# Kernel optimization log

Hardware: AMD Instinct MI355X
Metric: run time of the kernel (lower is better)

The kernel has to match this reference:

```python
import jax, jax.numpy as jnp
import numpy as np

WIN = 12          # max_relative_position
HEAD_DIM = 64     # E, equals num_units of relative-position tables


def _rel_embed(table, length):
    r = jnp.arange(length)
    idx = jnp.clip(r[None, :] - r[:, None], -WIN, WIN) + WIN  # [L, L]
    return table[idx]  # [L, L, E]


def setup_inputs() -> dict:
    key = jax.random.key(0)
    ks = jax.random.split(key, 7)
    B, L, H, E = 4, 1024, 8, HEAD_DIM
    shp = (B, L, H, E)
    xavier = float(np.sqrt(6.0 / (2 * WIN + 1 + E)))
    return {
        "x": jax.random.normal(ks[0], shp, jnp.float32),
        "y": jax.random.normal(ks[1], shp, jnp.float32),
        "v_x": jax.random.normal(ks[2], shp, jnp.float32),
        "v_y": jax.random.normal(ks[3], shp, jnp.float32),
        "rel_k_table": jax.random.uniform(ks[4], (2 * WIN + 1, E), jnp.float32, -xavier, xavier),
        "rel_vx_table": jax.random.uniform(ks[5], (2 * WIN + 1, E), jnp.float32, -xavier, xavier),
        "rel_vy_table": jax.random.uniform(ks[6], (2 * WIN + 1, E), jnp.float32, -xavier, xavier),
        "attn_mask1": jnp.zeros((1,), jnp.bool_),
        "attn_mask2": jnp.zeros((1,), jnp.bool_),
    }


def reference(x, y, v_x, v_y, rel_k_table, rel_vx_table, rel_vy_table, attn_mask1, attn_mask2):
    B, L, H, E = x.shape
    scale = 1.0 / float(np.sqrt(E))

    rel_k = _rel_embed(rel_k_table, L)    # [L, L, E]
    rel_vy = _rel_embed(rel_vy_table, L)  # [L, L, E]
    rel_vx = _rel_embed(rel_vx_table, L)  # [L, L, E]

    # scores1[b,h,l,s] = <x_bl h, y_bs h> + <x_bl h, rel_k[l,s]>
    scores1 = jnp.einsum('blhe,bshe->bhls', x, y) \
            + jnp.einsum('blhe,lse->bhls', x, rel_k)
    scores2 = jnp.swapaxes(scores1, -2, -1)  # pre-softmax transpose

    A1 = jax.nn.softmax(scale * scores1, axis=-1)  # [B,H,L,S]
    A2 = jax.nn.softmax(scale * scores2, axis=-1)

    V_Y = jnp.einsum('bhls,bshd->bhld', A1, v_y) \
        + jnp.einsum('bhls,lsd->bhld', A1, rel_vy)
    V_X = jnp.einsum('bhls,bshd->bhld', A2, v_x) \
        + jnp.einsum('bhls,lsd->bhld', A2, rel_vx)

    # module returns (V_Y^T, None, V_X^T, None); drop the Nones
    return jnp.swapaxes(V_Y, 1, 2), jnp.swapaxes(V_X, 1, 2)
```

## Files before the change

kernel.cpp:

```cpp
#include <hip/hip_runtime.h>
#include <math.h>

#define LQ 1024
#define RS 512
#define PJ 26
#define NP 32
#define ASCALE 0.18033688f

typedef __attribute__((ext_vector_type(4))) float f32x4;
typedef __attribute__((ext_vector_type(8))) short short8x;

__device__ __forceinline__ unsigned pk2(float a, float b) {
  unsigned r;
  asm("v_cvt_pk_bf16_f32 %0, %1, %2" : "=v"(r) : "v"(a), "v"(b));
  return r;
}

__device__ __forceinline__ int swz(int row, int bc) {
  return row * 128 + (bc ^ ((row & 7) << 4));
}
__device__ __forceinline__ int swzVT(int row, int bc) {
  return row * 128 + (bc ^ ((((row >> 3) ^ row) & 7) << 4));
}

__global__ __launch_bounds__(256) void k_relproj(const float* __restrict__ x,
                                                 const float* __restrict__ relk,
                                                 float* __restrict__ P) {
  __shared__ float rk[25][68];
  __shared__ float xs[64][68];
  const int tid = threadIdx.x;
  const int pair = blockIdx.y, l0 = blockIdx.x * 64;
  const int b = pair >> 3, h = pair & 7;
  for (int i = tid; i < 25 * 64; i += 256) rk[i >> 6][i & 63] = relk[i] * ASCALE;
  const int row = tid >> 2, q = tid & 3;
  const float* xr = x + (size_t)b * 524288 + (size_t)(l0 + row) * RS + h * 64 + q * 16;
#pragma unroll
  for (int i = 0; i < 4; ++i) {
    float4 a = *(const float4*)(xr + i * 4);
    xs[row][q * 16 + i * 4 + 0] = a.x; xs[row][q * 16 + i * 4 + 1] = a.y;
    xs[row][q * 16 + i * 4 + 2] = a.z; xs[row][q * 16 + i * 4 + 3] = a.w;
  }
  __syncthreads();
  float* Pr = P + ((size_t)pair * LQ + l0 + row) * PJ;
  for (int j = q; j < 25; j += 4) {
    float acc = 0.f;
#pragma unroll
    for (int e = 0; e < 64; ++e) acc += xs[row][e] * rk[j][e];
    Pr[j] = acc;
  }
}

__global__ __launch_bounds__(256, 2) void k_fused(
    const float* __restrict__ x, const float* __restrict__ y,
    const float* __restrict__ vx, const float* __restrict__ vy,
    const float* __restrict__ relvx, const float* __restrict__ relvy,
    const float* __restrict__ P_g, float* __restrict__ out_g) {
  __shared__ __align__(16) char U[16384];
  __shared__ __align__(16) char Bb[2][8192];
  __shared__ __align__(16) char Vb[2][8192];
  __shared__ float W[128 * PJ];

  const int tid = threadIdx.x;
  const int p = blockIdx.x;
  const int g = p & 63, bx = p >> 6;
  const int pair = g & 31, mode = g >> 5;
  const int b = pair >> 3, h = pair & 7;
  const int l0 = bx * 128;

  const float* Af = mode ? y : x;
  const float* Bl = mode ? x : y;
  const float* Vv = mode ? vx : vy;
  const float* tb = mode ? relvx : relvy;
  float* outp = out_g + (mode ? 2097152 : 0);

  const float* abase = Af + (size_t)b * 524288 + h * 64;
  const float* bbase = Bl + (size_t)b * 524288 + h * 64;
  const float* vbase = Vv + (size_t)b * 524288 + h * 64;
  const float* Pbase = P_g + (size_t)pair * LQ * PJ;
  float* outb = outp + (size_t)b * 524288 + h * 64;

  const int browA = tid >> 2, bqA = tid & 3;
  const int vsb = tid >> 4, vdb = tid & 15;

#pragma unroll
  for (int h2 = 0; h2 < 2; ++h2) {
    const float* s = abase + (size_t)(l0 + h2 * 64 + browA) * RS + bqA * 16;
#pragma unroll
    for (int hh = 0; hh < 2; ++hh) {
      float4 a = *(const float4*)(s + hh * 8);
      float4 c = *(const float4*)(s + hh * 8 + 4);
      uint4 u;
      u.x = pk2(a.x * ASCALE, a.y * ASCALE); u.y = pk2(a.z * ASCALE, a.w * ASCALE);
      u.z = pk2(c.x * ASCALE, c.y * ASCALE); u.w = pk2(c.z * ASCALE, c.w * ASCALE);
      *(uint4*)(U + swz(h2 * 64 + browA, bqA * 32 + hh * 16)) = u;
    }
  }
  {
    const float* sb2 = bbase + (size_t)browA * RS + bqA * 16;
#pragma unroll
    for (int hh = 0; hh < 2; ++hh) {
      float4 a = *(const float4*)(sb2 + hh * 8);
      float4 c = *(const float4*)(sb2 + hh * 8 + 4);
      uint4 u;
      u.x = pk2(a.x, a.y); u.y = pk2(a.z, a.w);
      u.z = pk2(c.x, c.y); u.w = pk2(c.z, c.w);
      *(uint4*)(Bb[0] + swz(browA, bqA * 32 + hh * 16)) = u;
    }
    const float* sv = vbase + (size_t)vsb * 4 * RS + vdb * 4;
    float4 r0 = *(const float4*)(sv);
    float4 r1 = *(const float4*)(sv + RS);
    float4 r2 = *(const float4*)(sv + 2 * RS);
    float4 r3 = *(const float4*)(sv + 3 * RS);
    uint2 w2;
    w2.x = pk2(r0.x, r1.x); w2.y = pk2(r2.x, r3.x);
    *(uint2*)(Vb[0] + swzVT(vdb * 4 + 0, vsb * 8)) = w2;
    w2.x = pk2(r0.y, r1.y); w2.y = pk2(r2.y, r3.y);
    *(uint2*)(Vb[0] + swzVT(vdb * 4 + 1, vsb * 8)) = w2;
    w2.x = pk2(r0.z, r1.z); w2.y = pk2(r2.z, r3.z);
    *(uint2*)(Vb[0] + swzVT(vdb * 4 + 2, vsb * 8)) = w2;
    w2.x = pk2(r0.w, r1.w); w2.y = pk2(r2.w, r3.w);
    *(uint2*)(Vb[0] + swzVT(vdb * 4 + 3, vsb * 8)) = w2;
  }
  for (int i = tid; i < 128 * PJ; i += 256) W[i] = 0.f;
  __syncthreads();

  const int lane = tid & 63, wv = tid >> 6;
  const int col16 = lane & 15, rg = lane >> 4;

  short8x af[2][2];
#pragma unroll
  for (int h2 = 0; h2 < 2; ++h2) {
    af[h2][0] = *(const short8x*)(U + swz(h2 * 64 + wv * 16 + col16, rg * 16));
    af[h2][1] = *(const short8x*)(U + swz(h2 * 64 + wv * 16 + col16, 64 + rg * 16));
  }

  const float* Prow[2];
  float bL[2] = {0.f, 0.f}, bR[2] = {0.f, 0.f};
#pragma unroll
  for (int h2 = 0; h2 < 2; ++h2)
    Prow[h2] = Pbase + (size_t)(l0 + h2 * 64 + wv * 16 + col16) * PJ;
  if (mode == 0) {
#pragma unroll
    for (int h2 = 0; h2 < 2; ++h2) { bL[h2] = Prow[h2][0]; bR[h2] = Prow[h2][24]; }
  }
  __syncthreads();

  f32x4 accO[2][4];
  float wl[2] = {0.f, 0.f}, wr[2] = {0.f, 0.f};
  const f32x4 z4 = {0.f, 0.f, 0.f, 0.f};
#pragma unroll
  for (int h2 = 0; h2 < 2; ++h2)
#pragma unroll
    for (int dt = 0; dt < 4; ++dt) accO[h2][dt] = z4;

  for (int t = 0; t < 16; ++t) {
    const int cb = t & 1, nb = cb ^ 1;
    const int relA = t * 64 - l0;
    const int relB = relA - 64;
    const bool fastA = (relA < -74 || relA > 74);
    const bool fastB = (relB < -74 || relB > 74);

    float4 pb[4], pv[4];
    if (t < 15) {
      const float* s = bbase + (size_t)((t + 1) * 64 + browA) * RS + bqA * 16;
#pragma unroll
      for (int i = 0; i < 4; ++i) pb[i] = *(const float4*)(s + i * 4);
      const float* sv2 = vbase + (size_t)((t + 1) * 64 + vsb * 4) * RS + vdb * 4;
#pragma unroll
      for (int k = 0; k < 4; ++k) pv[k] = *(const float4*)(sv2 + (size_t)k * RS);
    }

    float biasf[16];
    if (mode == 1 && (fastA || fastB)) {
      const bool right = fastA ? (relA > 0) : (relB > 0);
#pragma unroll
      for (int ct = 0; ct < 4; ++ct)
#pragma unroll
        for (int r = 0; r < 4; ++r)
          biasf[ct * 4 + r] =
              Pbase[(size_t)(t * 64 + ct * 16 + rg * 4 + r) * PJ + (right ? 0 : 24)];
    }

    f32x4 accS[2][4];
    const char* bB = Bb[cb];
#pragma unroll
    for (int ct = 0; ct < 4; ++ct) {
      short8x bf0 = *(const short8x*)(bB + swz(ct * 16 + col16, rg * 16));
      short8x bf1 = *(const short8x*)(bB + swz(ct * 16 + col16, 64 + rg * 16));
      f32x4 t0 = __builtin_amdgcn_mfma_f32_16x16x32_bf16(bf0, af[0][0], z4, 0, 0, 0);
      accS[0][ct] = __builtin_amdgcn_mfma_f32_16x16x32_bf16(bf1, af[0][1], t0, 0, 0, 0);
      f32x4 t1 = __builtin_amdgcn_mfma_f32_16x16x32_bf16(bf0, af[1][0], z4, 0, 0, 0);
      accS[1][ct] = __builtin_amdgcn_mfma_f32_16x16x32_bf16(bf1, af[1][1], t1, 0, 0, 0);
    }

#pragma unroll
    for (int h2 = 0; h2 < 2; ++h2) {
      const int rel = h2 ? relB : relA;
      const bool fast = h2 ? fastB : fastA;
      char* ea = U + (wv * 2 + h2) * 2048;
      if (fast) {
        const bool right = rel > 0;
        const float b0 = right ? bR[h2] : bL[h2];
#pragma unroll
        for (int ct = 0; ct < 4; ++ct) {
          float e0 = __builtin_exp2f(accS[h2][ct][0] + (mode ? biasf[ct * 4 + 0] : b0));
          float e1 = __builtin_exp2f(accS[h2][ct][1] + (mode ? biasf[ct * 4 + 1] : b0));
          float e2 = __builtin_exp2f(accS[h2][ct][2] + (mode ? biasf[ct * 4 + 2] : b0));
          float e3 = __builtin_exp2f(accS[h2][ct][3] + (mode ? biasf[ct * 4 + 3] : b0));
          float s4 = (e0 + e1) + (e2 + e3);
          if (right) wr[h2] += s4; else wl[h2] += s4;
          uint2 w2; w2.x = pk2(e0, e1); w2.y = pk2(e2, e3);
          *(uint2*)(ea + swz(col16, ct * 32 + rg * 8)) = w2;
        }
      } else {
#pragma unroll
        for (int ct = 0; ct < 4; ++ct) {
          float e[4];
#pragma unroll
          for (int r = 0; r < 4; ++r) {
            const int sl = ct * 16 + rg * 4 + r;
            const int d = rel + sl - (wv * 16 + col16);
            const int j = (d < -12 ? -12 : (d > 12 ? 12 : d)) + 12;
            const float bias = (mode == 0)
                ? Prow[h2][j]
                : Pbase[(size_t)(t * 64 + sl) * PJ + (24 - j)];
            e[r] = __builtin_exp2f(accS[h2][ct][r] + bias);
            if (d <= -12) wl[h2] += e[r];
            else if (d >= 12) wr[h2] += e[r];
            else W[(h2 * 64 + wv * 16 + col16) * PJ + (d + 12)] = e[r];
          }
          uint2 w2; w2.x = pk2(e[0], e[1]); w2.y = pk2(e[2], e[3]);
          *(uint2*)(ea + swz(col16, ct * 32 + rg * 8)) = w2;
        }
      }
    }

    __builtin_amdgcn_sched_barrier(0);
    asm volatile("s_waitcnt lgkmcnt(0)" ::: "memory");
    __builtin_amdgcn_sched_barrier(0);

    const char* vB = Vb[cb];
    short8x ef[2][2];
#pragma unroll
    for (int h2 = 0; h2 < 2; ++h2) {
      const char* ea = U + (wv * 2 + h2) * 2048;
      ef[h2][0] = *(const short8x*)(ea + swz(col16, rg * 16));
      ef[h2][1] = *(const short8x*)(ea + swz(col16, 64 + rg * 16));
    }
#pragma unroll
    for (int dt = 0; dt < 4; ++dt) {
      short8x v0 = *(const short8x*)(vB + swzVT(dt * 16 + col16, rg * 16));
      short8x v1 = *(const short8x*)(vB + swzVT(dt * 16 + col16, 64 + rg * 16));
      f32x4 t0 = __builtin_amdgcn_mfma_f32_16x16x32_bf16(ef[0][0], v0, accO[0][dt], 0, 0, 0);
      accO[0][dt] = __builtin_amdgcn_mfma_f32_16x16x32_bf16(ef[0][1], v1, t0, 0, 0, 0);
      f32x4 t1 = __builtin_amdgcn_mfma_f32_16x16x32_bf16(ef[1][0], v0, accO[1][dt], 0, 0, 0);
      accO[1][dt] = __builtin_amdgcn_mfma_f32_16x16x32_bf16(ef[1][1], v1, t1, 0, 0, 0);
    }

    if (t < 15) {
      uint4 u;
      u.x = pk2(pb[0].x, pb[0].y); u.y = pk2(pb[0].z, pb[0].w);
      u.z = pk2(pb[1].x, pb[1].y); u.w = pk2(pb[1].z, pb[1].w);
      *(uint4*)(Bb[nb] + swz(browA, bqA * 32)) = u;
      u.x = pk2(pb[2].x, pb[2].y); u.y = pk2(pb[2].z, pb[2].w);
      u.z = pk2(pb[3].x, pb[3].y); u.w = pk2(pb[3].z, pb[3].w);
      *(uint4*)(Bb[nb] + swz(browA, bqA * 32 + 16)) = u;
      uint2 w2;
      w2.x = pk2(pv[0].x, pv[1].x); w2.y = pk2(pv[2].x, pv[3].x);
      *(uint2*)(Vb[nb] + swzVT(vdb * 4 + 0, vsb * 8)) = w2;
      w2.x = pk2(pv[0].y, pv[1].y); w2.y = pk2(pv[2].y, pv[3].y);
      *(uint2*)(Vb[nb] + swzVT(vdb * 4 + 1, vsb * 8)) = w2;
      w2.x = pk2(pv[0].z, pv[1].z); w2.y = pk2(pv[2].z, pv[3].z);
      *(uint2*)(Vb[nb] + swzVT(vdb * 4 + 2, vsb * 8)) = w2;
      w2.x = pk2(pv[0].w, pv[1].w); w2.y = pk2(pv[2].w, pv[3].w);
      *(uint2*)(Vb[nb] + swzVT(vdb * 4 + 3, vsb * 8)) = w2;
    }
    __syncthreads();
  }

  float* tabf = (float*)U;
  for (int i = tid; i < 25 * 64; i += 256) tabf[i] = tb[i];
  __syncthreads();

  float wlR[2][4], wrR[2][4];
#pragma unroll
  for (int h2 = 0; h2 < 2; ++h2) {
    wl[h2] += __shfl_xor(wl[h2], 16); wl[h2] += __shfl_xor(wl[h2], 32);
    wr[h2] += __shfl_xor(wr[h2], 16); wr[h2] += __shfl_xor(wr[h2], 32);
#pragma unroll
    for (int r = 0; r < 4; ++r) {
      const int src = rg * 4 + r;
      wlR[h2][r] = __shfl(wl[h2], src);
      wrR[h2][r] = __shfl(wr[h2], src);
    }
  }

#pragma unroll
  for (int dt = 0; dt < 4; ++dt) {
    const int dd = dt * 16 + col16;
    const float t0 = tabf[dd], t24 = tabf[24 * 64 + dd];
#pragma unroll
    for (int h2 = 0; h2 < 2; ++h2)
#pragma unroll
      for (int r = 0; r < 4; ++r)
        accO[h2][dt][r] += wlR[h2][r] * t0 + wrR[h2][r] * t24;
  }
  float wsum[2][4] = {{0.f, 0.f, 0.f, 0.f}, {0.f, 0.f, 0.f, 0.f}};
#pragma unroll 4
  for (int j = 1; j < 24; ++j) {
    float tj[4];
#pragma unroll
    for (int dt = 0; dt < 4; ++dt) tj[dt] = tabf[j * 64 + dt * 16 + col16];
#pragma unroll
    for (int h2 = 0; h2 < 2; ++h2)
#pragma unroll
      for (int r = 0; r < 4; ++r) {
        const float w = W[(h2 * 64 + wv * 16 + rg * 4 + r) * PJ + j];
        wsum[h2][r] += w;
#pragma unroll
        for (int dt = 0; dt < 4; ++dt) accO[h2][dt][r] += w * tj[dt];
      }
  }
#pragma unroll
  for (int h2 = 0; h2 < 2; ++h2) {
    float inv[4];
#pragma unroll
    for (int r = 0; r < 4; ++r)
      inv[r] = 1.f / (wlR[h2][r] + wrR[h2][r] + wsum[h2][r]);
#pragma unroll
    for (int dt = 0; dt < 4; ++dt)
#pragma unroll
      for (int r = 0; r < 4; ++r) {
        const int row = h2 * 64 + wv * 16 + rg * 4 + r;
        outb[(size_t)(l0 + row) * RS + dt * 16 + col16] = accO[h2][dt][r] * inv[r];
      }
  }
}

extern "C" void kernel_launch(void* const* d_in, const int* in_sizes, int n_in,
                              void* d_out, int out_size, void* d_ws, size_t ws_size,
                              hipStream_t stream) {
  const float* x = (const float*)d_in[0];
  const float* y = (const float*)d_in[1];
  const float* vx = (const float*)d_in[2];
  const float* vy = (const float*)d_in[3];
  const float* relk = (const float*)d_in[4];
  const float* relvx = (const float*)d_in[5];
  const float* relvy = (const float*)d_in[6];
  float* out = (float*)d_out;

  float* P = (float*)d_ws;

  k_relproj<<<dim3(16, NP), 256, 0, stream>>>(x, relk, P);
  k_fused<<<dim3(512), 256, 0, stream>>>(x, y, vx, vy, relvx, relvy, P, out);
}
```

Baseline: 77.24 us.

## Software-pipeline QK MFMA one tile ahead with triple-buffered B/V staging

Restructures the main loop so the QK^T MFMAs for tile t+1 are issued before the softmax/exp work of tile t, ping-ponging two score accumulators. To support this, the B and V LDS staging goes from double to triple buffering, with global prefetch two tiles ahead. It also makes the left/right edge-weight accumulation branch-free in the slow path. The cost is more LDS (an extra 16 KB per block) and extra accumulator registers, which could reduce occupancy under the 2-blocks-per-CU launch bound.

```diff
diff --git a/kernel.cpp b/kernel.cpp
--- a/kernel.cpp
+++ b/kernel.cpp
@@ -56,8 +56,8 @@
     const float* __restrict__ relvx, const float* __restrict__ relvy,
     const float* __restrict__ P_g, float* __restrict__ out_g) {
   __shared__ __align__(16) char U[16384];
-  __shared__ __align__(16) char Bb[2][8192];
-  __shared__ __align__(16) char Vb[2][8192];
+  __shared__ __align__(16) char Bb[3][8192];
+  __shared__ __align__(16) char Vb[3][8192];
   __shared__ float W[128 * PJ];
 
   const int tid = threadIdx.x;
@@ -81,6 +81,35 @@
 
   const int browA = tid >> 2, bqA = tid & 3;
   const int vsb = tid >> 4, vdb = tid & 15;
+
+  auto stageB = [&](char* dst, int tile) {
+    const float* s = bbase + (size_t)(tile * 64 + browA) * RS + bqA * 16;
+#pragma unroll
+    for (int hh = 0; hh < 2; ++hh) {
+      float4 a = *(const float4*)(s + hh * 8);
+      float4 c = *(const float4*)(s + hh * 8 + 4);
+      uint4 u;
+      u.x = pk2(a.x, a.y); u.y = pk2(a.z, a.w);
+      u.z = pk2(c.x, c.y); u.w = pk2(c.z, c.w);
+      *(uint4*)(dst + swz(browA, bqA * 32 + hh * 16)) = u;
+    }
+  };
+  auto stageV = [&](char* dst, int tile) {
+    const float* sv = vbase + (size_t)(tile * 64 + vsb * 4) * RS + vdb * 4;
+    float4 r0 = *(const float4*)(sv);
+    float4 r1 = *(const float4*)(sv + RS);
+    float4 r2 = *(const float4*)(sv + 2 * RS);
+    float4 r3 = *(const float4*)(sv + 3 * RS);
+    uint2 w2;
+    w2.x = pk2(r0.x, r1.x); w2.y = pk2(r2.x, r3.x);
+    *(uint2*)(dst + swzVT(vdb * 4 + 0, vsb * 8)) = w2;
+    w2.x = pk2(r0.y, r1.y); w2.y = pk2(r2.y, r3.y);
+    *(uint2*)(dst + swzVT(vdb * 4 + 1, vsb * 8)) = w2;
+    w2.x = pk2(r0.z, r1.z); w2.y = pk2(r2.z, r3.z);
+    *(uint2*)(dst + swzVT(vdb * 4 + 2, vsb * 8)) = w2;
+    w2.x = pk2(r0.w, r1.w); w2.y = pk2(r2.w, r3.w);
+    *(uint2*)(dst + swzVT(vdb * 4 + 3, vsb * 8)) = w2;
+  };
 
 #pragma unroll
   for (int h2 = 0; h2 < 2; ++h2) {
@@ -95,32 +124,8 @@
       *(uint4*)(U + swz(h2 * 64 + browA, bqA * 32 + hh * 16)) = u;
     }
   }
-  {
-    const float* sb2 = bbase + (size_t)browA * RS + bqA * 16;
-#pragma unroll
-    for (int hh = 0; hh < 2; ++hh) {
-      float4 a = *(const float4*)(sb2 + hh * 8);
-      float4 c = *(const float4*)(sb2 + hh * 8 + 4);
-      uint4 u;
-      u.x = pk2(a.x, a.y); u.y = pk2(a.z, a.w);
-      u.z = pk2(c.x, c.y); u.w = pk2(c.z, c.w);
-      *(uint4*)(Bb[0] + swz(browA, bqA * 32 + hh * 16)) = u;
-    }
-    const float* sv = vbase + (size_t)vsb * 4 * RS + vdb * 4;
-    float4 r0 = *(const float4*)(sv);
-    float4 r1 = *(const float4*)(sv + RS);
-    float4 r2 = *(const float4*)(sv + 2 * RS);
-    float4 r3 = *(const float4*)(sv + 3 * RS);
-    uint2 w2;
-    w2.x = pk2(r0.x, r1.x); w2.y = pk2(r2.x, r3.x);
-    *(uint2*)(Vb[0] + swzVT(vdb * 4 + 0, vsb * 8)) = w2;
-    w2.x = pk2(r0.y, r1.y); w2.y = pk2(r2.y, r3.y);
-    *(uint2*)(Vb[0] + swzVT(vdb * 4 + 1, vsb * 8)) = w2;
-    w2.x = pk2(r0.z, r1.z); w2.y = pk2(r2.z, r3.z);
-    *(uint2*)(Vb[0] + swzVT(vdb * 4 + 2, vsb * 8)) = w2;
-    w2.x = pk2(r0.w, r1.w); w2.y = pk2(r2.w, r3.w);
-    *(uint2*)(Vb[0] + swzVT(vdb * 4 + 3, vsb * 8)) = w2;
-  }
+  stageB(Bb[0], 0); stageB(Bb[1], 1);
+  stageV(Vb[0], 0); stageV(Vb[1], 1);
   for (int i = tid; i < 128 * PJ; i += 256) W[i] = 0.f;
   __syncthreads();
 
@@ -133,7 +138,6 @@
     af[h2][0] = *(const short8x*)(U + swz(h2 * 64 + wv * 16 + col16, rg * 16));
     af[h2][1] = *(const short8x*)(U + swz(h2 * 64 + wv * 16 + col16, 64 + rg * 16));
   }
-
   const float* Prow[2];
   float bL[2] = {0.f, 0.f}, bR[2] = {0.f, 0.f};
 #pragma unroll
@@ -153,19 +157,31 @@
 #pragma unroll
     for (int dt = 0; dt < 4; ++dt) accO[h2][dt] = z4;
 
-  for (int t = 0; t < 16; ++t) {
-    const int cb = t & 1, nb = cb ^ 1;
+  auto qk = [&](const char* bB, f32x4 (&acc)[2][4]) {
+#pragma unroll
+    for (int ct = 0; ct < 4; ++ct) {
+      short8x bf0 = *(const short8x*)(bB + swz(ct * 16 + col16, rg * 16));
+      short8x bf1 = *(const short8x*)(bB + swz(ct * 16 + col16, 64 + rg * 16));
+      f32x4 t0 = __builtin_amdgcn_mfma_f32_16x16x32_bf16(bf0, af[0][0], z4, 0, 0, 0);
+      acc[0][ct] = __builtin_amdgcn_mfma_f32_16x16x32_bf16(bf1, af[0][1], t0, 0, 0, 0);
+      f32x4 t1 = __builtin_amdgcn_mfma_f32_16x16x32_bf16(bf0, af[1][0], z4, 0, 0, 0);
+      acc[1][ct] = __builtin_amdgcn_mfma_f32_16x16x32_bf16(bf1, af[1][1], t1, 0, 0, 0);
+    }
+  };
+
+  auto phase = [&](int t, f32x4 (&cur)[2][4], f32x4 (&nxt)[2][4]) {
+    const int ib0 = t % 3, ib1 = (t + 1) % 3, ib2 = (t + 2) % 3;
     const int relA = t * 64 - l0;
     const int relB = relA - 64;
     const bool fastA = (relA < -74 || relA > 74);
     const bool fastB = (relB < -74 || relB > 74);
 
     float4 pb[4], pv[4];
-    if (t < 15) {
-      const float* s = bbase + (size_t)((t + 1) * 64 + browA) * RS + bqA * 16;
+    if (t + 2 < 16) {
+      const float* s = bbase + (size_t)((t + 2) * 64 + browA) * RS + bqA * 16;
 #pragma unroll
       for (int i = 0; i < 4; ++i) pb[i] = *(const float4*)(s + i * 4);
-      const float* sv2 = vbase + (size_t)((t + 1) * 64 + vsb * 4) * RS + vdb * 4;
+      const float* sv2 = vbase + (size_t)((t + 2) * 64 + vsb * 4) * RS + vdb * 4;
 #pragma unroll
       for (int k = 0; k < 4; ++k) pv[k] = *(const float4*)(sv2 + (size_t)k * RS);
     }
@@ -181,17 +197,7 @@
               Pbase[(size_t)(t * 64 + ct * 16 + rg * 4 + r) * PJ + (right ? 0 : 24)];
     }
 
-    f32x4 accS[2][4];
-    const char* bB = Bb[cb];
-#pragma unroll
-    for (int ct = 0; ct < 4; ++ct) {
-      short8x bf0 = *(const short8x*)(bB + swz(ct * 16 + col16, rg * 16));
-      short8x bf1 = *(const short8x*)(bB + swz(ct * 16 + col16, 64 + rg * 16));
-      f32x4 t0 = __builtin_amdgcn_mfma_f32_16x16x32_bf16(bf0, af[0][0], z4, 0, 0, 0);
-      accS[0][ct] = __builtin_amdgcn_mfma_f32_16x16x32_bf16(bf1, af[0][1], t0, 0, 0, 0);
-      f32x4 t1 = __builtin_amdgcn_mfma_f32_16x16x32_bf16(bf0, af[1][0], z4, 0, 0, 0);
-      accS[1][ct] = __builtin_amdgcn_mfma_f32_16x16x32_bf16(bf1, af[1][1], t1, 0, 0, 0);
-    }
+    if (t + 1 < 16) qk(Bb[ib1], nxt);
 
 #pragma unroll
     for (int h2 = 0; h2 < 2; ++h2) {
@@ -203,10 +209,10 @@
         const float b0 = right ? bR[h2] : bL[h2];
 #pragma unroll
         for (int ct = 0; ct < 4; ++ct) {
-          float e0 = __builtin_exp2f(accS[h2][ct][0] + (mode ? biasf[ct * 4 + 0] : b0));
-          float e1 = __builtin_exp2f(accS[h2][ct][1] + (mode ? biasf[ct * 4 + 1] : b0));
-          float e2 = __builtin_exp2f(accS[h2][ct][2] + (mode ? biasf[ct * 4 + 2] : b0));
-          float e3 = __builtin_exp2f(accS[h2][ct][3] + (mode ? biasf[ct * 4 + 3] : b0));
+          float e0 = __builtin_exp2f(cur[h2][ct][0] + (mode ? biasf[ct * 4 + 0] : b0));
+          float e1 = __builtin_exp2f(cur[h2][ct][1] + (mode ? biasf[ct * 4 + 1] : b0));
+          float e2 = __builtin_exp2f(cur[h2][ct][2] + (mode ? biasf[ct * 4 + 2] : b0));
+          float e3 = __builtin_exp2f(cur[h2][ct][3] + (mode ? biasf[ct * 4 + 3] : b0));
           float s4 = (e0 + e1) + (e2 + e3);
           if (right) wr[h2] += s4; else wl[h2] += s4;
           uint2 w2; w2.x = pk2(e0, e1); w2.y = pk2(e2, e3);
@@ -215,7 +221,7 @@
       } else {
 #pragma unroll
         for (int ct = 0; ct < 4; ++ct) {
-          float e[4];
+          float e[4], el[4], er[4];
 #pragma unroll
           for (int r = 0; r < 4; ++r) {
             const int sl = ct * 16 + rg * 4 + r;
@@ -224,11 +230,15 @@
             const float bias = (mode == 0)
                 ? Prow[h2][j]
                 : Pbase[(size_t)(t * 64 + sl) * PJ + (24 - j)];
-            e[r] = __builtin_exp2f(accS[h2][ct][r] + bias);
-            if (d <= -12) wl[h2] += e[r];
-            else if (d >= 12) wr[h2] += e[r];
-            else W[(h2 * 64 + wv * 16 + col16) * PJ + (d + 12)] = e[r];
+            e[r] = __builtin_exp2f(cur[h2][ct][r] + bias);
+            const bool isl = (d <= -12), isr = (d >= 12);
+            el[r] = isl ? e[r] : 0.f;
+            er[r] = isr ? e[r] : 0.f;
+            if (!isl && !isr)
+              W[(h2 * 64 + wv * 16 + col16) * PJ + (d + 12)] = e[r];
           }
+          wl[h2] += (el[0] + el[1]) + (el[2] + el[3]);
+          wr[h2] += (er[0] + er[1]) + (er[2] + er[3]);
           uint2 w2; w2.x = pk2(e[0], e[1]); w2.y = pk2(e[2], e[3]);
           *(uint2*)(ea + swz(col16, ct * 32 + rg * 8)) = w2;
         }
@@ -239,7 +249,7 @@
     asm volatile("s_waitcnt lgkmcnt(0)" ::: "memory");
     __builtin_amdgcn_sched_barrier(0);
 
-    const char* vB = Vb[cb];
+    const char* vB = Vb[ib0];
     short8x ef[2][2];
 #pragma unroll
     for (int h2 = 0; h2 < 2; ++h2) {
@@ -257,25 +267,32 @@
       accO[1][dt] = __builtin_amdgcn_mfma_f32_16x16x32_bf16(ef[1][1], v1, t1, 0, 0, 0);
     }
 
-    if (t < 15) {
+    if (t + 2 < 16) {
       uint4 u;
       u.x = pk2(pb[0].x, pb[0].y); u.y = pk2(pb[0].z, pb[0].w);
       u.z = pk2(pb[1].x, pb[1].y); u.w = pk2(pb[1].z, pb[1].w);
-      *(uint4*)(Bb[nb] + swz(browA, bqA * 32)) = u;
+      *(uint4*)(Bb[ib2] + swz(browA, bqA * 32)) = u;
       u.x = pk2(pb[2].x, pb[2].y); u.y = pk2(pb[2].z, pb[2].w);
       u.z = pk2(pb[3].x, pb[3].y); u.w = pk2(pb[3].z, pb[3].w);
-      *(uint4*)(Bb[nb] + swz(browA, bqA * 32 + 16)) = u;
+      *(uint4*)(Bb[ib2] + swz(browA, bqA * 32 + 16)) = u;
       uint2 w2;
       w2.x = pk2(pv[0].x, pv[1].x); w2.y = pk2(pv[2].x, pv[3].x);
-      *(uint2*)(Vb[nb] + swzVT(vdb * 4 + 0, vsb * 8)) = w2;
+      *(uint2*)(Vb[ib2] + swzVT(vdb * 4 + 0, vsb * 8)) = w2;
       w2.x = pk2(pv[0].y, pv[1].y); w2.y = pk2(pv[2].y, pv[3].y);
-      *(uint2*)(Vb[nb] + swzVT(vdb * 4 + 1, vsb * 8)) = w2;
+      *(uint2*)(Vb[ib2] + swzVT(vdb * 4 + 1, vsb * 8)) = w2;
       w2.x = pk2(pv[0].z, pv[1].z); w2.y = pk2(pv[2].z, pv[3].z);
-      *(uint2*)(Vb[nb] + swzVT(vdb * 4 + 2, vsb * 8)) = w2;
+      *(uint2*)(Vb[ib2] + swzVT(vdb * 4 + 2, vsb * 8)) = w2;
       w2.x = pk2(pv[0].w, pv[1].w); w2.y = pk2(pv[2].w, pv[3].w);
-      *(uint2*)(Vb[nb] + swzVT(vdb * 4 + 3, vsb * 8)) = w2;
+      *(uint2*)(Vb[ib2] + swzVT(vdb * 4 + 3, vsb * 8)) = w2;
     }
     __syncthreads();
+  };
+
+  f32x4 accA[2][4], accB[2][4];
+  qk(Bb[0], accA);
+  for (int i = 0; i < 8; ++i) {
+    phase(2 * i, accA, accB);
+    phase(2 * i + 1, accB, accA);
   }
 
   float* tabf = (float*)U;
```

After: 109.9 us. 1.42x slower.
